# Optimization experiments

Hardware: AMD Instinct MI355X
Metric: run time of the kernel (lower is better)

## Reference

```python
import jax, jax.numpy as jnp
import numpy as np

B, S, D, H = 2, 4096, 1024, 16
DK = D // H


def setup_inputs() -> dict:
    key = jax.random.key(0)
    ks = jax.random.split(key, 7)
    sc = 1.0 / np.sqrt(D)
    return {
        "q": jax.random.normal(ks[0], (B, S, D), jnp.float32),
        "k": jax.random.normal(ks[1], (B, S, D), jnp.float32),
        "v": jax.random.normal(ks[2], (B, S, D), jnp.float32),
        "wq": jax.random.normal(ks[3], (D, D), jnp.float32) * sc,
        "wk": jax.random.normal(ks[4], (D, D), jnp.float32) * sc,
        "wv": jax.random.normal(ks[5], (D, D), jnp.float32) * sc,
        "w0": jax.random.normal(ks[6], (D, D), jnp.float32) * sc,
    }


def reference(q, k, v, wq, wk, wv, w0):
    # Linear(bias=False): y = x @ W^T  (torch convention, W is [out,in])
    qp = jnp.einsum('bsd,ed->bse', q, wq).reshape(B, S, H, DK).transpose(0, 2, 1, 3)
    kp = jnp.einsum('bsd,ed->bse', k, wk).reshape(B, S, H, DK).transpose(0, 2, 1, 3)
    vp = jnp.einsum('bsd,ed->bse', v, wv).reshape(B, S, H, DK).transpose(0, 2, 1, 3)
    scale = 1.0 / jnp.sqrt(jnp.float32(DK))
    att = jnp.einsum('bhqd,bhkd->bhqk', qp, kp) * scale  # [B,H,S,S]
    att = jax.nn.softmax(att, axis=-1)
    x = jnp.einsum('bhqk,bhkd->bhqd', att, vp)  # [B,H,S,DK]
    x = x.transpose(0, 2, 1, 3).reshape(B, S, D)
    out = jnp.einsum('bsd,ed->bse', x, w0)
    return out
```

## Files before the change

kernel.cpp:

```cpp
#include <hip/hip_runtime.h>
#include <hip/hip_bf16.h>
#include <stdint.h>

#define Bb 2
#define Ss 4096
#define Dd 1024
#define Hh 16
#define DKk 64

typedef __attribute__((ext_vector_type(8))) short bf16x8;
typedef __attribute__((ext_vector_type(4))) float f32x4;
typedef __attribute__((ext_vector_type(16))) float f32x16;

#define MFMA16(a, b, c) __builtin_amdgcn_mfma_f32_32x32x16_bf16(a, b, c, 0, 0, 0)

__device__ __forceinline__ unsigned short f2bf(float f) {
    union { float f; unsigned int u; } x; x.f = f;
    return (unsigned short)((x.u + 0x7fffu + ((x.u >> 16) & 1u)) >> 16);
}

__device__ __forceinline__ void gload16(const void* g, void* l) {
    __builtin_amdgcn_global_load_lds(
        (const __attribute__((address_space(1))) void*)g,
        (__attribute__((address_space(3))) void*)l, 16, 0, 0);
}

__global__ __launch_bounds__(256) void cvt_all(const float* __restrict__ q, const float* __restrict__ k,
                                               const float* __restrict__ v, const float* __restrict__ wq,
                                               const float* __restrict__ wk, const float* __restrict__ wv,
                                               const float* __restrict__ w0, unsigned short* __restrict__ ws) {
    const int QKV4 = 3 * 2097152;
    const int TOT4 = QKV4 + 4 * 262144;
    int i = blockIdx.x * 256 + threadIdx.x;
    const int stride = gridDim.x * 256;
    ushort4* out = (ushort4*)ws;
    for (; i < TOT4; i += stride) {
        const float4* src;
        int di;
        if (i < QKV4) {
            const int r = i >> 21;
            const float* s = r == 0 ? q : (r == 1 ? k : v);
            src = (const float4*)s + (i & 2097151);
            di = i;
        } else {
            const int j = i - QKV4;
            const int r = j >> 18;
            const float* s = r == 0 ? wq : (r == 1 ? wk : (r == 2 ? wv : w0));
            src = (const float4*)s + (j & 262143);
            di = i + 2097152;
        }
        const float4 vv = *src;
        ushort4 o;
        o.x = f2bf(vv.x); o.y = f2bf(vv.y); o.z = f2bf(vv.z); o.w = f2bf(vv.w);
        out[di] = o;
    }
}

template <int MODE>
__global__ __launch_bounds__(256) void gemm_bt(const unsigned short* __restrict__ A,
                                               const unsigned short* __restrict__ W,
                                               void* __restrict__ Y) {
    __shared__ unsigned short As[128 * 32];
    __shared__ unsigned short Bs[128 * 32];
    const int t = threadIdx.x;
    const int wid = t >> 6, lane = t & 63, q4 = lane >> 4, l16 = lane & 15;
    const int wr = wid >> 1, wc = wid & 1;
    const int arow0 = blockIdx.x * 128;
    const int wrow0 = blockIdx.y * 128;
    f32x4 acc[4][4] = {};
    for (int kt = 0; kt < 1024; kt += 32) {
        __syncthreads();
#pragma unroll
        for (int i = 0; i < 2; i++) {
            const int o = i * 4096 + t * 16;
            const int r = o >> 6, c = (o & 63) >> 1;
            gload16(A + (long)(arow0 + r) * 1024 + kt + c, (char*)As + o);
            gload16(W + (long)(wrow0 + r) * 1024 + kt + c, (char*)Bs + o);
        }
        __syncthreads();
        bf16x8 a[4], b[4];
#pragma unroll
        for (int m = 0; m < 4; m++)
            a[m] = *(const bf16x8*)((const char*)As + (wr * 64 + m * 16 + l16) * 64 + q4 * 16);
#pragma unroll
        for (int n = 0; n < 4; n++)
            b[n] = *(const bf16x8*)((const char*)Bs + (wc * 64 + n * 16 + l16) * 64 + q4 * 16);
#pragma unroll
        for (int m = 0; m < 4; m++)
#pragma unroll
            for (int n = 0; n < 4; n++)
                acc[m][n] = __builtin_amdgcn_mfma_f32_16x16x32_bf16(a[m], b[n], acc[m][n], 0, 0, 0);
    }
    const int rb = arow0 + wr * 64, cb = wrow0 + wc * 64;
#pragma unroll
    for (int m = 0; m < 4; m++)
#pragma unroll
        for (int n = 0; n < 4; n++)
#pragma unroll
            for (int r = 0; r < 4; r++) {
                const int row = rb + m * 16 + q4 * 4 + r;
                const int col = cb + n * 16 + l16;
                const float v = acc[m][n][r];
                if (MODE == 0) {
                    ((unsigned short*)Y)[(long)row * 1024 + col] = f2bf(v);
                } else if (MODE == 1) {
                    const int bb = row >> 12, s = row & 4095;
                    const int hh = col >> 6, dk = col & 63;
                    ((unsigned short*)Y)[(((long)(bb * Hh + hh) * DKk + dk) << 12) + s] = f2bf(v);
                } else {
                    ((float*)Y)[(long)row * 1024 + col] = v;
                }
            }
}

__global__ __launch_bounds__(256, 4) void attn_fwd(const unsigned short* __restrict__ qp,
                                                   const unsigned short* __restrict__ kp,
                                                   const unsigned short* __restrict__ vt,
                                                   unsigned short* __restrict__ xo) {
    __shared__ __align__(16) char smem[32768];
    const int t = threadIdx.x;
    const int wid = t >> 6, lane = t & 63;
    const int l5 = lane & 31;
    const int ihi = lane >> 5;
    const int e5 = l5 & 7;
    const int qt = blockIdx.x, h = blockIdx.y, b = blockIdx.z;
    const unsigned short* qbase = qp + ((long)b * Ss + qt * 128) * Dd + h * 64;
    const unsigned short* kbase = kp + (long)b * Ss * Dd + h * 64;
    const unsigned short* vbase = vt + (long)(b * Hh + h) * DKk * Ss;
    char* Qs = smem + 16384;

#pragma unroll
    for (int i = 0; i < 4; i++) {
        const int o = i * 4096 + t * 16;
        const int r = o >> 7;
        const int c = ((o & 127) ^ ((r & 7) << 4)) >> 1;
        gload16(qbase + (long)r * Dd + c, Qs + o);
    }
    const int o0 = t * 16;
    const int r0 = o0 >> 7;
    const int c0 = ((o0 & 127) ^ ((r0 & 7) << 4)) >> 1;
    const unsigned short* ksrc = kbase + (long)r0 * Dd + c0;
    const unsigned short* vsrc = vbase + (long)r0 * Ss + c0;
    gload16(ksrc,             smem + o0);
    gload16(ksrc + 32 * Dd,   smem + 4096 + o0);
    gload16(vsrc,             smem + 8192 + o0);
    gload16(vsrc + 32 * Ss,   smem + 12288 + o0);
    __syncthreads();

    const int qrow = wid * 32 + l5;
    bf16x8 bQ[4];
#pragma unroll
    for (int m = 0; m < 4; m++) {
        const int slot = (m * 2 + ihi) ^ (qrow & 7);
        bQ[m] = *(const bf16x8*)(Qs + qrow * 128 + (slot << 4));
    }
    __syncthreads();
    gload16(ksrc + 64 * Dd,        smem + 16384 + o0);
    gload16(ksrc + 96 * Dd,        smem + 20480 + o0);
    gload16(vsrc + 64,             smem + 24576 + o0);
    gload16(vsrc + 32 * Ss + 64,   smem + 28672 + o0);
    const unsigned short* pk = ksrc + 128 * Dd;
    const unsigned short* pv = vsrc + 128;

    int adm[4];
#pragma unroll
    for (int m = 0; m < 4; m++)
        adm[m] = l5 * 128 + ((((m * 2 + ihi) ^ e5)) << 4);

    const float c1f = 0.1803368801111244f;
    float mi = -1e30f, li = 0.f;
    f32x16 accO[2] = {};

    for (int kt2 = 0; kt2 < 64; kt2 += 2) {
#pragma unroll
        for (int hf = 0; hf < 2; hf++) {
            const int kt = kt2 + hf;
            const int BO = hf << 14;
            const char* Kc = smem + BO;
            const char* Vc = smem + BO + 8192;
            f32x16 accS[2] = {};
            __builtin_amdgcn_s_setprio(1);
#pragma unroll
            for (int m = 0; m < 4; m++) {
                const bf16x8 aK0 = *(const bf16x8*)(Kc + adm[m]);
                const bf16x8 aK1 = *(const bf16x8*)(Kc + 4096 + adm[m]);
                accS[0] = MFMA16(aK0, bQ[m], accS[0]);
                accS[1] = MFMA16(aK1, bQ[m], accS[1]);
            }
            __builtin_amdgcn_s_setprio(0);
            float mx0[8];
#pragma unroll
            for (int r = 0; r < 8; r++)
                mx0[r] = fmaxf(accS[0][r], accS[0][r + 8]);
#pragma unroll
            for (int r = 0; r < 8; r++)
                mx0[r] = fmaxf(mx0[r], fmaxf(accS[1][r], accS[1][r + 8]));
            float m4a = fmaxf(fmaxf(mx0[0], mx0[1]), fmaxf(mx0[2], mx0[3]));
            float m4b = fmaxf(fmaxf(mx0[4], mx0[5]), fmaxf(mx0[6], mx0[7]));
            float rmx = fmaxf(m4a, m4b);
            if (!__all(rmx * c1f <= mi + 8.f)) {
                const float r2 = fmaxf(rmx, __shfl_xor(rmx, 32, 64));
                const float mn = fmaxf(mi, r2 * c1f);
                const float alpha = __builtin_amdgcn_exp2f(mi - mn);
                mi = mn;
                li *= alpha;
#pragma unroll
                for (int d = 0; d < 2; d++)
#pragma unroll
                    for (int r = 0; r < 16; r++) accO[d][r] *= alpha;
            }
            unsigned pwu[2][4][2];
            float ps = 0.f;
#pragma unroll
            for (int kb = 0; kb < 2; kb++)
#pragma unroll
                for (int s = 0; s < 4; s++)
#pragma unroll
                    for (int w = 0; w < 2; w++) {
                        const float p0 = __builtin_amdgcn_exp2f(fmaf(accS[kb][4 * s + 2 * w],     c1f, -mi));
                        const float p1 = __builtin_amdgcn_exp2f(fmaf(accS[kb][4 * s + 2 * w + 1], c1f, -mi));
                        ps += p0 + p1;
                        asm("v_cvt_pk_bf16_f32 %0, %1, %2" : "=v"(pwu[kb][s][w]) : "v"(p0), "v"(p1));
                    }
            ps += __shfl_xor(ps, 32, 64);
            li += ps;
            __builtin_amdgcn_s_setprio(1);
#pragma unroll
            for (int m = 0; m < 4; m++) {
                const int kb = m >> 1, s0 = (m & 1) * 2;
                unsigned x0 = pwu[kb][s0][0], y0 = pwu[kb][s0 + 1][0];
                unsigned x1 = pwu[kb][s0][1], y1 = pwu[kb][s0 + 1][1];
                asm("v_permlane32_swap_b32 %0, %1" : "+v"(x0), "+v"(y0));
                asm("v_permlane32_swap_b32 %0, %1" : "+v"(x1), "+v"(y1));
                union { unsigned u[4]; bf16x8 v; } fr;
                fr.u[0] = x0; fr.u[1] = x1; fr.u[2] = y0; fr.u[3] = y1;
#pragma unroll
                for (int dblk = 0; dblk < 2; dblk++) {
                    const bf16x8 aV = *(const bf16x8*)(Vc + dblk * 4096 + adm[m]);
                    accO[dblk] = MFMA16(aV, fr.v, accO[dblk]);
                }
            }
            __builtin_amdgcn_s_setprio(0);
            __syncthreads();
            if (kt < 62) {
                char* dst = smem + BO;
                gload16(pk,            dst + o0);
                gload16(pk + 32 * Dd,  dst + 4096 + o0);
                gload16(pv,            dst + 8192 + o0);
                gload16(pv + 32 * Ss,  dst + 12288 + o0);
                pk += 64 * Dd;
                pv += 64;
            }
        }
    }

    const float rli = 1.0f / li;
    const int erow = wid * 32 + l5;
#pragma unroll
    for (int dblk = 0; dblk < 2; dblk++)
#pragma unroll
        for (int tt = 0; tt < 8; tt++) {
            const unsigned short b0 = f2bf(accO[dblk][2 * tt] * rli);
            const unsigned short b1 = f2bf(accO[dblk][2 * tt + 1] * rli);
            const int slot = (dblk * 4 + (tt >> 1)) ^ e5;
            const int phys = erow * 128 + (slot << 4) + ihi * 8 + (tt & 1) * 4;
            *(unsigned*)(smem + phys) = ((unsigned)b1 << 16) | b0;
        }
    __syncthreads();
#pragma unroll
    for (int p = 0; p < 4; p++) {
        const int o = p * 4096 + t * 16;
        const int row = o >> 7;
        const int slot = (o & 127) >> 4;
        const uint4 val = *(const uint4*)(smem + row * 128 + ((slot ^ (row & 7)) << 4));
        *(uint4*)((char*)(xo + ((long)b * Ss + qt * 128 + row) * Dd + h * 64) + slot * 16) = val;
    }
}

extern "C" void kernel_launch(void* const* d_in, const int* in_sizes, int n_in,
                              void* d_out, int out_size, void* d_ws, size_t ws_size,
                              hipStream_t stream) {
    const float* q  = (const float*)d_in[0];
    const float* k  = (const float*)d_in[1];
    const float* v  = (const float*)d_in[2];
    const float* wq = (const float*)d_in[3];
    const float* wk = (const float*)d_in[4];
    const float* wv = (const float*)d_in[5];
    const float* w0 = (const float*)d_in[6];

    unsigned short* ws = (unsigned short*)d_ws;
    const long NE = (long)Bb * Ss * Dd;
    unsigned short* qb  = ws;
    unsigned short* kb  = ws + NE;
    unsigned short* vb  = ws + 2 * NE;
    unsigned short* x1  = ws + 3 * NE;
    unsigned short* wqb = ws + 4 * NE;
    unsigned short* wkb = wqb + 1048576;
    unsigned short* wvb = wkb + 1048576;
    unsigned short* w0b = wvb + 1048576;

    cvt_all<<<2048, 256, 0, stream>>>(q, k, v, wq, wk, wv, w0, ws);

    dim3 gg(64, 8);
    gemm_bt<0><<<gg, 256, 0, stream>>>(qb, wqb, x1);
    gemm_bt<0><<<gg, 256, 0, stream>>>(kb, wkb, qb);
    gemm_bt<1><<<gg, 256, 0, stream>>>(vb, wvb, kb);
    dim3 ga(32, 16, 2);
    attn_fwd<<<ga, 256, 0, stream>>>(x1, qb, kb, vb);
    gemm_bt<2><<<gg, 256, 0, stream>>>(vb, w0b, (float*)d_out);
}
```

Measured before the change: 306.7 us.

## Replace syncthreads with partial vmcnt waits and restructure softmax reductions

Replaces __syncthreads in the attention kernel with explicit s_waitcnt vmcnt(N) plus s_barrier. Each wait then only drains the older in-flight global-to-LDS loads, so the prefetch of the next K/V tile keeps overlapping with compute. The row-max reduction is rewritten as chains of three-input max so the compiler can emit v_max3. The row-sum is split into four independent accumulators to shorten the dependency chain. This adds an extra barrier per iteration and relies on hand-counted vmcnt values being correct for memory ordering.

```diff
diff --git a/kernel.cpp b/kernel.cpp
--- a/kernel.cpp
+++ b/kernel.cpp
@@ -23,6 +23,10 @@
     __builtin_amdgcn_global_load_lds(
         (const __attribute__((address_space(1))) void*)g,
         (__attribute__((address_space(3))) void*)l, 16, 0, 0);
+}
+
+__device__ __forceinline__ float max3f(float a, float b, float c) {
+    return fmaxf(fmaxf(a, b), c);
 }
 
 __global__ __launch_bounds__(256) void cvt_all(const float* __restrict__ q, const float* __restrict__ k,
@@ -145,7 +149,9 @@
     gload16(ksrc + 32 * Dd,   smem + 4096 + o0);
     gload16(vsrc,             smem + 8192 + o0);
     gload16(vsrc + 32 * Ss,   smem + 12288 + o0);
-    __syncthreads();
+    asm volatile("s_waitcnt vmcnt(4)" ::: "memory");
+    __builtin_amdgcn_s_barrier();
+    asm volatile("" ::: "memory");
 
     const int qrow = wid * 32 + l5;
     bf16x8 bQ[4];
@@ -154,13 +160,18 @@
         const int slot = (m * 2 + ihi) ^ (qrow & 7);
         bQ[m] = *(const bf16x8*)(Qs + qrow * 128 + (slot << 4));
     }
-    __syncthreads();
+    asm volatile("s_waitcnt lgkmcnt(0)" ::: "memory");
+    __builtin_amdgcn_s_barrier();
+    asm volatile("" ::: "memory");
     gload16(ksrc + 64 * Dd,        smem + 16384 + o0);
     gload16(ksrc + 96 * Dd,        smem + 20480 + o0);
     gload16(vsrc + 64,             smem + 24576 + o0);
     gload16(vsrc + 32 * Ss + 64,   smem + 28672 + o0);
     const unsigned short* pk = ksrc + 128 * Dd;
     const unsigned short* pv = vsrc + 128;
+    asm volatile("s_waitcnt vmcnt(4)" ::: "memory");
+    __builtin_amdgcn_s_barrier();
+    asm volatile("" ::: "memory");
 
     int adm[4];
 #pragma unroll
@@ -188,16 +199,23 @@
                 accS[1] = MFMA16(aK1, bQ[m], accS[1]);
             }
             __builtin_amdgcn_s_setprio(0);
-            float mx0[8];
-#pragma unroll
-            for (int r = 0; r < 8; r++)
-                mx0[r] = fmaxf(accS[0][r], accS[0][r + 8]);
-#pragma unroll
-            for (int r = 0; r < 8; r++)
-                mx0[r] = fmaxf(mx0[r], fmaxf(accS[1][r], accS[1][r + 8]));
-            float m4a = fmaxf(fmaxf(mx0[0], mx0[1]), fmaxf(mx0[2], mx0[3]));
-            float m4b = fmaxf(fmaxf(mx0[4], mx0[5]), fmaxf(mx0[6], mx0[7]));
-            float rmx = fmaxf(m4a, m4b);
+            float m0 = max3f(accS[0][0], accS[0][1], accS[0][2]);
+            m0 = max3f(m0, accS[0][3], accS[0][4]);
+            m0 = max3f(m0, accS[0][5], accS[0][6]);
+            m0 = fmaxf(m0, accS[0][7]);
+            float m1 = max3f(accS[0][8], accS[0][9], accS[0][10]);
+            m1 = max3f(m1, accS[0][11], accS[0][12]);
+            m1 = max3f(m1, accS[0][13], accS[0][14]);
+            m1 = fmaxf(m1, accS[0][15]);
+            float m2 = max3f(accS[1][0], accS[1][1], accS[1][2]);
+            m2 = max3f(m2, accS[1][3], accS[1][4]);
+            m2 = max3f(m2, accS[1][5], accS[1][6]);
+            m2 = fmaxf(m2, accS[1][7]);
+            float m3 = max3f(accS[1][8], accS[1][9], accS[1][10]);
+            m3 = max3f(m3, accS[1][11], accS[1][12]);
+            m3 = max3f(m3, accS[1][13], accS[1][14]);
+            m3 = fmaxf(m3, accS[1][15]);
+            const float rmx = fmaxf(max3f(m0, m1, m2), m3);
             if (!__all(rmx * c1f <= mi + 8.f)) {
                 const float r2 = fmaxf(rmx, __shfl_xor(rmx, 32, 64));
                 const float mn = fmaxf(mi, r2 * c1f);
@@ -210,7 +228,7 @@
                     for (int r = 0; r < 16; r++) accO[d][r] *= alpha;
             }
             unsigned pwu[2][4][2];
-            float ps = 0.f;
+            float psa[4] = {0.f, 0.f, 0.f, 0.f};
 #pragma unroll
             for (int kb = 0; kb < 2; kb++)
 #pragma unroll
@@ -219,9 +237,10 @@
                     for (int w = 0; w < 2; w++) {
                         const float p0 = __builtin_amdgcn_exp2f(fmaf(accS[kb][4 * s + 2 * w],     c1f, -mi));
                         const float p1 = __builtin_amdgcn_exp2f(fmaf(accS[kb][4 * s + 2 * w + 1], c1f, -mi));
-                        ps += p0 + p1;
+                        psa[kb * 2 + w] += p0 + p1;
                         asm("v_cvt_pk_bf16_f32 %0, %1, %2" : "=v"(pwu[kb][s][w]) : "v"(p0), "v"(p1));
                     }
+            float ps = (psa[0] + psa[1]) + (psa[2] + psa[3]);
             ps += __shfl_xor(ps, 32, 64);
             li += ps;
             __builtin_amdgcn_s_setprio(1);
@@ -241,7 +260,8 @@
                 }
             }
             __builtin_amdgcn_s_setprio(0);
-            __syncthreads();
+            __builtin_amdgcn_s_barrier();
+            asm volatile("" ::: "memory");
             if (kt < 62) {
                 char* dst = smem + BO;
                 gload16(pk,            dst + o0);
@@ -250,7 +270,12 @@
                 gload16(pv + 32 * Ss,  dst + 12288 + o0);
                 pk += 64 * Dd;
                 pv += 64;
-            }
+                asm volatile("s_waitcnt vmcnt(4)" ::: "memory");
+            } else {
+                asm volatile("s_waitcnt vmcnt(0)" ::: "memory");
+            }
+            __builtin_amdgcn_s_barrier();
+            asm volatile("" ::: "memory");
         }
     }
 
```

Result: no change. 304.8 us (-0.6%).
